# Performance work log

Measured on AMD Instinct MI355X. Metric: run time of the kernel, lower is better.

Reference implementation:

```python
import jax, jax.numpy as jnp
import numpy as np
from jax import lax

N_NODES = 10000
N_EDGES = 320000


def setup_inputs() -> dict:
    key = jax.random.key(0)
    ks = jax.random.split(key, 7)
    B, H, N, F = 4, 24, N_NODES, 32
    hid = 64
    x = jax.random.normal(ks[0], (B, H, N, F), dtype=jnp.float32)
    mask = jax.random.uniform(ks[1], (B, H), dtype=jnp.float32)
    edge_index = jax.random.randint(ks[2], (2, N_EDGES), 0, N, dtype=jnp.int32)
    W1 = jax.random.normal(ks[3], (F + 1, hid), dtype=jnp.float32) * (1.0 / np.sqrt(F + 1))
    b1 = jax.random.normal(ks[4], (hid,), dtype=jnp.float32) * 0.02
    W2 = jax.random.normal(ks[5], (hid, F), dtype=jnp.float32) * (1.0 / np.sqrt(hid))
    b2 = jax.random.normal(ks[6], (F,), dtype=jnp.float32) * 0.02
    return {"x": x, "mask": mask, "edge_index": edge_index,
            "W1": W1, "b1": b1, "W2": W2, "b2": b2}


def _gcn_norm(edge_index, num_nodes):
    # PyG GCNConv default: add self loops, symmetric normalization.
    loops = jnp.arange(num_nodes, dtype=edge_index.dtype)
    src = jnp.concatenate([edge_index[0], loops])
    dst = jnp.concatenate([edge_index[1], loops])
    deg = jax.ops.segment_sum(jnp.ones_like(dst, dtype=jnp.float32), dst,
                              num_segments=num_nodes)
    dinv = jnp.where(deg > 0, lax.rsqrt(jnp.maximum(deg, 1e-12)), 0.0)
    norm = dinv[src] * dinv[dst]  # [E']
    return src, dst, norm


def reference(x, mask, edge_index, W1, b1, W2, b2):
    B, H, N, F = x.shape
    src, dst, norm = _gcn_norm(edge_index, N)

    def gcn(h, W, b):
        # h: [B, N, Fin] -> lin, then normalized neighbor aggregation, then bias
        hw = h @ W                                   # [B, N, Fout]
        msg = hw[:, src, :].transpose(1, 0, 2)       # [E', B, Fout]
        msg = msg * norm[:, None, None]
        agg = jax.ops.segment_sum(msg, dst, num_segments=N)  # [N, B, Fout]
        return agg.transpose(1, 0, 2) + b

    def per_hour(carry, inp):
        xh, mh = inp                                 # xh: [B, N, F], mh: [B]
        mc = jnp.broadcast_to(mh[:, None, None], (B, N, 1))
        h = jnp.concatenate([xh, mc], axis=-1)       # [B, N, F+1]
        out = jnp.tanh(gcn(gcn(h, W1, b1), W2, b2))  # [B, N, F]
        return carry, out

    _, outs = lax.scan(per_hour, None,
                       (x.transpose(1, 0, 2, 3), mask.T))  # [H, B, N, F]
    return outs.transpose(1, 0, 2, 3)                     # [B, H, N, F]
```

## Files before the change

### kernel.cpp

```cpp
#include <hip/hip_runtime.h>
#include <hip/hip_fp16.h>

#define NN 10000
#define FF 32
#define PG 4
#define NGRP 24

typedef __attribute__((ext_vector_type(2))) float f32x2;

__device__ __forceinline__ unsigned short f2h(float f){
  union { unsigned short s; _Float16 h; } c; c.h = (_Float16)f; return c.s;
}

__device__ __forceinline__ void fmix2p(float& ax, float& ay, unsigned wpk, unsigned h){
  asm("v_fma_mix_f32 %0, %2, %3, %0 op_sel_hi:[1,1,0]\n\t"
      "v_fma_mix_f32 %1, %2, %3, %1 op_sel:[0,1,0] op_sel_hi:[1,1,0]"
      : "+v"(ax), "+v"(ay) : "s"(wpk), "v"(h));
}
__device__ __forceinline__ void fmix2s(float& ax, float& ay, float w, unsigned h){
  asm("v_fma_mix_f32 %0, %2, %3, %0 op_sel_hi:[0,1,0]\n\t"
      "v_fma_mix_f32 %1, %2, %3, %1 op_sel:[0,1,0] op_sel_hi:[0,1,0]"
      : "+v"(ax), "+v"(ay) : "s"(w), "v"(h));
}

__device__ __forceinline__ void pkfma(f32x2& acc, f32x2 w, f32x2 x){
  asm("v_pk_fma_f32 %0, %1, %2, %0" : "+v"(acc) : "s"(w), "v"(x));
}

__global__ void k_count(const int* __restrict__ dst, int* __restrict__ cnt,
                        unsigned* __restrict__ csr, int csrcap, int E){
  int e = blockIdx.x * 256 + threadIdx.x;
  if (e >= E) return;
  csr[e] = 0u;
  int e2 = e + E;
  if (e2 < csrcap) csr[e2] = 0u;
  atomicAdd(&cnt[dst[e]], 1);
}

__global__ __launch_bounds__(256) void k_prep(const int* __restrict__ cnt,
    int2* __restrict__ oe, float* __restrict__ dinv, int* __restrict__ gtop,
    const float* __restrict__ W1, const float* __restrict__ W2,
    const float* __restrict__ b1, float* __restrict__ W12, float* __restrict__ bb){
  int bx = blockIdx.x, tid = threadIdx.x;
  if (bx < 40){
    int i = bx * 256 + tid;
    if (i < NN){
      int c = cnt[i];
      int pad = (c + 3) & ~3;
      int start = atomicAdd(gtop, pad);
      oe[i] = make_int2(start, start + pad);
      dinv[i] = rsqrtf((float)(c + 1));
    }
  } else {
    int j = (bx - 40) * 256 + tid;
    if (j < 33 * 32){
      int k = j >> 5, c = j & 31;
      float s = 0.f;
      for (int m = 0; m < 64; ++m) s += W1[k * 64 + m] * W2[m * 32 + c];
      W12[j] = s;
    } else if (j < 33 * 32 + 32){
      int c = j - 33 * 32;
      float s = 0.f;
      for (int m = 0; m < 64; ++m) s += b1[m] * W2[m * 32 + c];
      bb[c] = s;
    }
  }
}

__global__ void k_scatter(const int* __restrict__ ei, const int2* __restrict__ oe,
                          int* __restrict__ cur, const float* __restrict__ dinv,
                          unsigned* __restrict__ csr, float* __restrict__ srow, int E){
  int e = blockIdx.x * 256 + threadIdx.x;
  if (e >= E) return;
  int s = ei[e], d = ei[E + e];
  float ds = dinv[s];
  int pos = oe[d].x + atomicAdd(&cur[d], 1);
  csr[pos] = ((unsigned)s << 16) | (unsigned)f2h(ds);
  atomicAdd(&srow[d], ds);
}

__global__ __launch_bounds__(256) void k_gemm1(const float* __restrict__ x,
    const float* __restrict__ mask, const float* __restrict__ W12,
    unsigned* __restrict__ hw){
  __shared__ float xs[256][32];
  const int pg = blockIdx.y;
  const int n0 = blockIdx.x * 256;
  const int t  = threadIdx.x;
  const int l  = t & 63;
  const int wv = __builtin_amdgcn_readfirstlane(t) >> 6;
  const int grp = pg >> 2, p = pg & 3;
  const float mv = mask[pg];
  const f32x2* Wp = (const f32x2*)W12;
  f32x2 acc[16];
  #pragma unroll
  for (int qf = 0; qf < 16; ++qf){
    f32x2 w = Wp[32 * 16 + qf];
    acc[qf].x = mv * w.x; acc[qf].y = mv * w.y;
  }
  const int rsub = l >> 3;
  const int qd   = (l & 7) ^ rsub;
  const float* xpg = x + (size_t)pg * (NN * FF);
  #pragma unroll
  for (int i = 0; i < 8; ++i){
    int chunk = wv * 8 + i;
    int grow = n0 + chunk * 8 + rsub;
    grow = grow < NN ? grow : NN - 1;
    const float* gsrc = xpg + (size_t)grow * FF + (qd << 2);
    char* ldst = (char*)&xs[0][0] + (chunk << 10);
    __builtin_amdgcn_global_load_lds(
        (const __attribute__((address_space(1))) void*)gsrc,
        (__attribute__((address_space(3))) void*)ldst, 16, 0, 0);
  }
  asm volatile("s_waitcnt vmcnt(0)" ::: "memory");
  __syncthreads();
  const int n = n0 + t;
  if (n >= NN) return;
  const int sw = (t & 7) << 2;
  #pragma unroll
  for (int Q = 0; Q < 8; ++Q){
    float4 v = *(const float4*)&xs[t][(Q << 2) ^ sw];
    const float* vf = (const float*)&v;
    #pragma unroll
    for (int j = 0; j < 4; ++j){
      int k = (Q << 2) + j;
      f32x2 xk2; xk2.x = vf[j]; xk2.y = vf[j];
      #pragma unroll
      for (int qf = 0; qf < 16; ++qf) pkfma(acc[qf], Wp[k * 16 + qf], xk2);
    }
  }
  unsigned* hwg = hw + (size_t)grp * (NN * 64) + ((size_t)n << 6) + (p << 4);
  #pragma unroll
  for (int j = 0; j < 4; ++j){
    uint4 u;
    u.x = (unsigned)f2h(acc[4*j+0].x) | ((unsigned)f2h(acc[4*j+0].y) << 16);
    u.y = (unsigned)f2h(acc[4*j+1].x) | ((unsigned)f2h(acc[4*j+1].y) << 16);
    u.z = (unsigned)f2h(acc[4*j+2].x) | ((unsigned)f2h(acc[4*j+2].y) << 16);
    u.w = (unsigned)f2h(acc[4*j+3].x) | ((unsigned)f2h(acc[4*j+3].y) << 16);
    ((uint4*)hwg)[j] = u;
  }
}

__device__ __forceinline__ void map_block(int bx, int& grp, int& chunk){
  int r  = bx / 5000;
  int w8 = bx % 5000;
  grp   = r * 8 + (w8 & 7);
  chunk = w8 >> 3;
}

#define ROWB(w) ((((unsigned)(w)) >> 8) & 0xFFFF00u)
__device__ __forceinline__ void agg_edges(int e0, int e1,
    const unsigned* __restrict__ csr, const char* __restrict__ Vb, int loff,
    float& ax, float& ay){
  int nq = (e1 - e0) >> 2;
  if (nq <= 0) return;
  const int4* c4 = (const int4*)(csr + e0);
  const int qlast = nq - 1;
  #define VLD(w) (*(const unsigned*)(Vb + (unsigned)(ROWB(w) + loff)))
  int4 cA, cB, cC, cD;
  int4 cA2, cB2, cC2, cD2;
  int4 cA3, cB3, cC3, cD3;
  unsigned rA0,rA1,rA2,rA3, rB0,rB1,rB2,rB3;
  unsigned rC0,rC1,rC2,rC3, rD0,rD1,rD2,rD3;
  {
    int i1 = 1<=qlast?1:qlast, i2 = 2<=qlast?2:qlast, i3 = 3<=qlast?3:qlast;
    cA = c4[0]; cB = c4[i1]; cC = c4[i2]; cD = c4[i3];
    int i4 = 4<=qlast?4:qlast, i5 = 5<=qlast?5:qlast;
    int i6 = 6<=qlast?6:qlast, i7 = 7<=qlast?7:qlast;
    cA2 = c4[i4]; cB2 = c4[i5]; cC2 = c4[i6]; cD2 = c4[i7];
    int i8 = 8<=qlast?8:qlast, i9 = 9<=qlast?9:qlast;
    int i10 = 10<=qlast?10:qlast, i11 = 11<=qlast?11:qlast;
    cA3 = c4[i8]; cB3 = c4[i9]; cC3 = c4[i10]; cD3 = c4[i11];
    rA0 = VLD(cA.x); rA1 = VLD(cA.y); rA2 = VLD(cA.z); rA3 = VLD(cA.w);
    rB0 = VLD(cB.x); rB1 = VLD(cB.y); rB2 = VLD(cB.z); rB3 = VLD(cB.w);
    rC0 = VLD(cC.x); rC1 = VLD(cC.y); rC2 = VLD(cC.z); rC3 = VLD(cC.w);
    rD0 = VLD(cD.x); rD1 = VLD(cD.y); rD2 = VLD(cD.z); rD3 = VLD(cD.w);
  }
  int q = 0;
  #define AGG_STEP(cX, cX2, cX3, r0, r1, r2, r3)                        \
    do {                                                                \
      fmix2p(ax, ay, (unsigned)cX.x, r0);                               \
      fmix2p(ax, ay, (unsigned)cX.y, r1);                               \
      fmix2p(ax, ay, (unsigned)cX.z, r2);                               \
      fmix2p(ax, ay, (unsigned)cX.w, r3);                               \
      r0 = VLD(cX2.x); r1 = VLD(cX2.y);                                 \
      r2 = VLD(cX2.z); r3 = VLD(cX2.w);                                 \
      cX = cX2; cX2 = cX3;                                              \
    } while (0)
  for (; q + 3 < nq; q += 4){
    AGG_STEP(cA, cA2, cA3, rA0,rA1,rA2,rA3);
    AGG_STEP(cB, cB2, cB3, rB0,rB1,rB2,rB3);
    AGG_STEP(cC, cC2, cC3, rC0,rC1,rC2,rC3);
    AGG_STEP(cD, cD2, cD3, rD0,rD1,rD2,rD3);
    int j0 = q+12 <= qlast ? q+12 : qlast;
    int j1 = q+13 <= qlast ? q+13 : qlast;
    int j2 = q+14 <= qlast ? q+14 : qlast;
    int j3 = q+15 <= qlast ? q+15 : qlast;
    cA3 = c4[j0]; cB3 = c4[j1]; cC3 = c4[j2]; cD3 = c4[j3];
  }
  #undef AGG_STEP
  #undef VLD
  int rem = nq - q;
  if (rem > 0){
    fmix2p(ax, ay, (unsigned)cA.x, rA0);
    fmix2p(ax, ay, (unsigned)cA.y, rA1);
    fmix2p(ax, ay, (unsigned)cA.z, rA2);
    fmix2p(ax, ay, (unsigned)cA.w, rA3);
  }
  if (rem > 1){
    fmix2p(ax, ay, (unsigned)cB.x, rB0);
    fmix2p(ax, ay, (unsigned)cB.y, rB1);
    fmix2p(ax, ay, (unsigned)cB.z, rB2);
    fmix2p(ax, ay, (unsigned)cB.w, rB3);
  }
  if (rem > 2){
    fmix2p(ax, ay, (unsigned)cC.x, rC0);
    fmix2p(ax, ay, (unsigned)cC.y, rC1);
    fmix2p(ax, ay, (unsigned)cC.z, rC2);
    fmix2p(ax, ay, (unsigned)cC.w, rC3);
  }
}

__global__ __launch_bounds__(256) void k_agg1(const int2* __restrict__ oe,
    const unsigned* __restrict__ csr, const float* __restrict__ dinv,
    const unsigned int* __restrict__ V, unsigned int* __restrict__ T){
  int grp, chunk; map_block(blockIdx.x, grp, chunk);
  int tid = threadIdx.x;
  int l = tid & 63;
  int wv = __builtin_amdgcn_readfirstlane(tid) >> 6;
  const char* Vb = (const char*)(V + (size_t)grp * (NN * 64));
  unsigned int* Tg = T + (size_t)grp * (NN * 64);
  int loff = l * 4;
  for (int it = 0; it < 4; ++it){
    int n = chunk * 16 + wv * 4 + it;
    float din = dinv[n];
    int2 ee = oe[n];
    unsigned sv = *(const unsigned*)(Vb + (unsigned)((n << 8) + loff));
    float ax = 0.f, ay = 0.f;
    fmix2s(ax, ay, din, sv);
    agg_edges(ee.x, ee.y, csr, Vb, loff, ax, ay);
    Tg[((size_t)n << 6) + l] =
        (unsigned)f2h(din * ax) | ((unsigned)f2h(din * ay) << 16);
  }
}

__global__ __launch_bounds__(256) void k_agg2(const int2* __restrict__ oe,
    const unsigned* __restrict__ csr, const float* __restrict__ dinv,
    const float* __restrict__ srow, const float* __restrict__ bb,
    const float* __restrict__ b2, const unsigned int* __restrict__ V,
    float* __restrict__ out){
  int grp, chunk; map_block(blockIdx.x, grp, chunk);
  int tid = threadIdx.x;
  int l = tid & 63;
  int wv = __builtin_amdgcn_readfirstlane(tid) >> 6;
  int p = l >> 4, fi = l & 15;
  const char* Vb = (const char*)(V + (size_t)grp * (NN * 64));
  int pg = grp * PG + p;
  float2 bbq = ((const float2*)bb)[fi];
  float2 b2q = ((const float2*)b2)[fi];
  float* outp = out + (size_t)pg * (NN * FF);
  int loff = l * 4;
  for (int it = 0; it < 4; ++it){
    int n = chunk * 16 + wv * 4 + it;
    float din = dinv[n];
    int2 ee = oe[n];
    unsigned sv = *(const unsigned*)(Vb + (unsigned)((n << 8) + loff));
    float ax = 0.f, ay = 0.f;
    fmix2s(ax, ay, din, sv);
    agg_edges(ee.x, ee.y, csr, Vb, loff, ax, ay);
    float sr = din * (din + srow[n]);
    float2 o;
    o.x = tanhf(din * ax + sr * bbq.x + b2q.x);
    o.y = tanhf(din * ay + sr * bbq.y + b2q.y);
    ((float2*)(outp + (size_t)n * FF))[fi] = o;
  }
}

extern "C" void kernel_launch(void* const* d_in, const int* in_sizes, int n_in,
                              void* d_out, int out_size, void* d_ws, size_t ws_size,
                              hipStream_t stream){
  const float* x    = (const float*)d_in[0];
  const float* mask = (const float*)d_in[1];
  const int*   ei   = (const int*)d_in[2];
  const float* W1   = (const float*)d_in[3];
  const float* b1   = (const float*)d_in[4];
  const float* W2   = (const float*)d_in[5];
  const float* b2   = (const float*)d_in[6];
  float* out = (float*)d_out;
  const int E = in_sizes[2] / 2;
  const int CSRCAP = E + 3 * NN + 64;

  char* wsp = (char*)d_ws;
  auto alloc = [&](size_t bytes) -> char* {
    char* p = wsp; wsp += (bytes + 255) & ~(size_t)255; return p;
  };
  int*   cnt  = (int*)  alloc((size_t)NN * 4);
  int*   cur  = (int*)  alloc((size_t)NN * 4);
  float* srow = (float*)alloc((size_t)NN * 4);
  int*   gtop = (int*)  alloc(256);
  float* dinv = (float*)alloc((size_t)NN * 4);
  int2*  oe   = (int2*) alloc((size_t)NN * 8);
  float* W12  = (float*)alloc(33 * 32 * 4);
  float* bbv  = (float*)alloc(32 * 4);
  unsigned* csr = (unsigned*)alloc((size_t)CSRCAP * 4);
  const size_t per_group = (size_t)NN * 64 * 4;
  unsigned int* hw = (unsigned int*)alloc((size_t)NGRP * per_group);
  unsigned int* t1 = (unsigned int*)alloc((size_t)NGRP * per_group);

  size_t zspan = (size_t)((char*)dinv - (char*)cnt);
  hipMemsetAsync(cnt, 0, zspan, stream);
  k_count  <<<(E + 255) / 256, 256, 0, stream>>>(ei + E, cnt, csr, CSRCAP, E);
  k_prep   <<<45, 256, 0, stream>>>(cnt, oe, dinv, gtop, W1, W2, b1, W12, bbv);
  k_scatter<<<(E + 255) / 256, 256, 0, stream>>>(ei, oe, cur, dinv, csr, srow, E);

  k_gemm1<<<dim3(40, 96), 256, 0, stream>>>(x, mask, W12, hw);
  k_agg1 <<<15000, 256, 0, stream>>>(oe, csr, dinv, hw, t1);
  k_agg2 <<<15000, 256, 0, stream>>>(oe, csr, dinv, srow, bbv, b2, t1, out);
}
```

Before: 492.1 us.

## Split edge lists across wave halves with 8-byte gathers and shuffle reduction

The aggregation kernels now split each node's edge list between the two 32-lane halves of a wave. Each half handles alternating edges and each lane gathers 8 bytes (two packed half2 values) instead of 4, and the two halves are combined with a cross-lane shuffle. This halves the number of gather instructions per edge and widens each memory access. The costs are that edge weights must sit in VGPRs instead of SGPRs, there are extra shuffles, and half the lanes sit idle during the output store.

Result: slower. 600.6 us (+22.1%).

```diff
diff --git a/kernel.cpp b/kernel.cpp
--- a/kernel.cpp
+++ b/kernel.cpp
@@ -12,15 +12,15 @@
   union { unsigned short s; _Float16 h; } c; c.h = (_Float16)f; return c.s;
 }
 
-__device__ __forceinline__ void fmix2p(float& ax, float& ay, unsigned wpk, unsigned h){
+__device__ __forceinline__ void fmix2v(float& ax, float& ay, unsigned wpk, unsigned h){
   asm("v_fma_mix_f32 %0, %2, %3, %0 op_sel_hi:[1,1,0]\n\t"
       "v_fma_mix_f32 %1, %2, %3, %1 op_sel:[0,1,0] op_sel_hi:[1,1,0]"
-      : "+v"(ax), "+v"(ay) : "s"(wpk), "v"(h));
-}
-__device__ __forceinline__ void fmix2s(float& ax, float& ay, float w, unsigned h){
+      : "+v"(ax), "+v"(ay) : "v"(wpk), "v"(h));
+}
+__device__ __forceinline__ void fmix2(float& ax, float& ay, float w, unsigned h){
   asm("v_fma_mix_f32 %0, %2, %3, %0 op_sel_hi:[0,1,0]\n\t"
       "v_fma_mix_f32 %1, %2, %3, %1 op_sel:[0,1,0] op_sel_hi:[0,1,0]"
-      : "+v"(ax), "+v"(ay) : "s"(w), "v"(h));
+      : "+v"(ax), "+v"(ay) : "v"(w), "v"(h));
 }
 
 __device__ __forceinline__ void pkfma(f32x2& acc, f32x2 w, f32x2 x){
@@ -150,47 +150,53 @@
 #define ROWB(w) ((((unsigned)(w)) >> 8) & 0xFFFF00u)
 __device__ __forceinline__ void agg_edges(int e0, int e1,
     const unsigned* __restrict__ csr, const char* __restrict__ Vb, int loff,
-    float& ax, float& ay){
+    bool hi, float& ax0, float& ay0, float& ax1, float& ay1){
   int nq = (e1 - e0) >> 2;
   if (nq <= 0) return;
   const int4* c4 = (const int4*)(csr + e0);
   const int qlast = nq - 1;
-  #define VLD(w) (*(const unsigned*)(Vb + (unsigned)(ROWB(w) + loff)))
-  int4 cA, cB, cC, cD;
+  #define V2LD(w) (*(const uint2*)(Vb + (unsigned)(ROWB(w) + loff)))
   int4 cA2, cB2, cC2, cD2;
   int4 cA3, cB3, cC3, cD3;
-  unsigned rA0,rA1,rA2,rA3, rB0,rB1,rB2,rB3;
-  unsigned rC0,rC1,rC2,rC3, rD0,rD1,rD2,rD3;
+  unsigned wA0,wA1, wB0,wB1, wC0,wC1, wD0,wD1;
+  uint2 rA0,rA1, rB0,rB1, rC0,rC1, rD0,rD1;
   {
     int i1 = 1<=qlast?1:qlast, i2 = 2<=qlast?2:qlast, i3 = 3<=qlast?3:qlast;
-    cA = c4[0]; cB = c4[i1]; cC = c4[i2]; cD = c4[i3];
+    int4 cA = c4[0], cB = c4[i1], cC = c4[i2], cD = c4[i3];
+    wA0 = hi ? (unsigned)cA.y : (unsigned)cA.x;
+    wA1 = hi ? (unsigned)cA.w : (unsigned)cA.z;
+    wB0 = hi ? (unsigned)cB.y : (unsigned)cB.x;
+    wB1 = hi ? (unsigned)cB.w : (unsigned)cB.z;
+    wC0 = hi ? (unsigned)cC.y : (unsigned)cC.x;
+    wC1 = hi ? (unsigned)cC.w : (unsigned)cC.z;
+    wD0 = hi ? (unsigned)cD.y : (unsigned)cD.x;
+    wD1 = hi ? (unsigned)cD.w : (unsigned)cD.z;
+    rA0 = V2LD(wA0); rA1 = V2LD(wA1);
+    rB0 = V2LD(wB0); rB1 = V2LD(wB1);
+    rC0 = V2LD(wC0); rC1 = V2LD(wC1);
+    rD0 = V2LD(wD0); rD1 = V2LD(wD1);
     int i4 = 4<=qlast?4:qlast, i5 = 5<=qlast?5:qlast;
     int i6 = 6<=qlast?6:qlast, i7 = 7<=qlast?7:qlast;
     cA2 = c4[i4]; cB2 = c4[i5]; cC2 = c4[i6]; cD2 = c4[i7];
     int i8 = 8<=qlast?8:qlast, i9 = 9<=qlast?9:qlast;
     int i10 = 10<=qlast?10:qlast, i11 = 11<=qlast?11:qlast;
     cA3 = c4[i8]; cB3 = c4[i9]; cC3 = c4[i10]; cD3 = c4[i11];
-    rA0 = VLD(cA.x); rA1 = VLD(cA.y); rA2 = VLD(cA.z); rA3 = VLD(cA.w);
-    rB0 = VLD(cB.x); rB1 = VLD(cB.y); rB2 = VLD(cB.z); rB3 = VLD(cB.w);
-    rC0 = VLD(cC.x); rC1 = VLD(cC.y); rC2 = VLD(cC.z); rC3 = VLD(cC.w);
-    rD0 = VLD(cD.x); rD1 = VLD(cD.y); rD2 = VLD(cD.z); rD3 = VLD(cD.w);
   }
   int q = 0;
-  #define AGG_STEP(cX, cX2, cX3, r0, r1, r2, r3)                        \
+  #define AGG_STEP(w0, w1, r0, r1, cX2, cX3)                            \
     do {                                                                \
-      fmix2p(ax, ay, (unsigned)cX.x, r0);                               \
-      fmix2p(ax, ay, (unsigned)cX.y, r1);                               \
-      fmix2p(ax, ay, (unsigned)cX.z, r2);                               \
-      fmix2p(ax, ay, (unsigned)cX.w, r3);                               \
-      r0 = VLD(cX2.x); r1 = VLD(cX2.y);                                 \
-      r2 = VLD(cX2.z); r3 = VLD(cX2.w);                                 \
-      cX = cX2; cX2 = cX3;                                              \
+      fmix2v(ax0, ay0, w0, r0.x); fmix2v(ax1, ay1, w0, r0.y);           \
+      fmix2v(ax0, ay0, w1, r1.x); fmix2v(ax1, ay1, w1, r1.y);           \
+      w0 = hi ? (unsigned)cX2.y : (unsigned)cX2.x;                      \
+      w1 = hi ? (unsigned)cX2.w : (unsigned)cX2.z;                      \
+      r0 = V2LD(w0); r1 = V2LD(w1);                                     \
+      cX2 = cX3;                                                        \
     } while (0)
   for (; q + 3 < nq; q += 4){
-    AGG_STEP(cA, cA2, cA3, rA0,rA1,rA2,rA3);
-    AGG_STEP(cB, cB2, cB3, rB0,rB1,rB2,rB3);
-    AGG_STEP(cC, cC2, cC3, rC0,rC1,rC2,rC3);
-    AGG_STEP(cD, cD2, cD3, rD0,rD1,rD2,rD3);
+    AGG_STEP(wA0, wA1, rA0, rA1, cA2, cA3);
+    AGG_STEP(wB0, wB1, rB0, rB1, cB2, cB3);
+    AGG_STEP(wC0, wC1, rC0, rC1, cC2, cC3);
+    AGG_STEP(wD0, wD1, rD0, rD1, cD2, cD3);
     int j0 = q+12 <= qlast ? q+12 : qlast;
     int j1 = q+13 <= qlast ? q+13 : qlast;
     int j2 = q+14 <= qlast ? q+14 : qlast;
@@ -198,25 +204,19 @@
     cA3 = c4[j0]; cB3 = c4[j1]; cC3 = c4[j2]; cD3 = c4[j3];
   }
   #undef AGG_STEP
-  #undef VLD
+  #undef V2LD
   int rem = nq - q;
   if (rem > 0){
-    fmix2p(ax, ay, (unsigned)cA.x, rA0);
-    fmix2p(ax, ay, (unsigned)cA.y, rA1);
-    fmix2p(ax, ay, (unsigned)cA.z, rA2);
-    fmix2p(ax, ay, (unsigned)cA.w, rA3);
+    fmix2v(ax0, ay0, wA0, rA0.x); fmix2v(ax1, ay1, wA0, rA0.y);
+    fmix2v(ax0, ay0, wA1, rA1.x); fmix2v(ax1, ay1, wA1, rA1.y);
   }
   if (rem > 1){
-    fmix2p(ax, ay, (unsigned)cB.x, rB0);
-    fmix2p(ax, ay, (unsigned)cB.y, rB1);
-    fmix2p(ax, ay, (unsigned)cB.z, rB2);
-    fmix2p(ax, ay, (unsigned)cB.w, rB3);
+    fmix2v(ax0, ay0, wB0, rB0.x); fmix2v(ax1, ay1, wB0, rB0.y);
+    fmix2v(ax0, ay0, wB1, rB1.x); fmix2v(ax1, ay1, wB1, rB1.y);
   }
   if (rem > 2){
-    fmix2p(ax, ay, (unsigned)cC.x, rC0);
-    fmix2p(ax, ay, (unsigned)cC.y, rC1);
-    fmix2p(ax, ay, (unsigned)cC.z, rC2);
-    fmix2p(ax, ay, (unsigned)cC.w, rC3);
+    fmix2v(ax0, ay0, wC0, rC0.x); fmix2v(ax1, ay1, wC0, rC0.y);
+    fmix2v(ax0, ay0, wC1, rC1.x); fmix2v(ax1, ay1, wC1, rC1.y);
   }
 }
 
@@ -225,21 +225,30 @@
     const unsigned int* __restrict__ V, unsigned int* __restrict__ T){
   int grp, chunk; map_block(blockIdx.x, grp, chunk);
   int tid = threadIdx.x;
-  int l = tid & 63;
+  int l = tid & 63, j = l & 31;
+  bool hi = l >= 32;
   int wv = __builtin_amdgcn_readfirstlane(tid) >> 6;
   const char* Vb = (const char*)(V + (size_t)grp * (NN * 64));
   unsigned int* Tg = T + (size_t)grp * (NN * 64);
-  int loff = l * 4;
+  int loff = j * 8;
   for (int it = 0; it < 4; ++it){
     int n = chunk * 16 + wv * 4 + it;
     float din = dinv[n];
     int2 ee = oe[n];
-    unsigned sv = *(const unsigned*)(Vb + (unsigned)((n << 8) + loff));
-    float ax = 0.f, ay = 0.f;
-    fmix2s(ax, ay, din, sv);
-    agg_edges(ee.x, ee.y, csr, Vb, loff, ax, ay);
-    Tg[((size_t)n << 6) + l] =
-        (unsigned)f2h(din * ax) | ((unsigned)f2h(din * ay) << 16);
+    uint2 sv = *(const uint2*)(Vb + (unsigned)((n << 8) + loff));
+    float ax0 = 0.f, ay0 = 0.f, ax1 = 0.f, ay1 = 0.f;
+    float wself = hi ? 0.f : din;
+    fmix2(ax0, ay0, wself, sv.x);
+    fmix2(ax1, ay1, wself, sv.y);
+    agg_edges(ee.x, ee.y, csr, Vb, loff, hi, ax0, ay0, ax1, ay1);
+    ax0 += __shfl_xor(ax0, 32); ay0 += __shfl_xor(ay0, 32);
+    ax1 += __shfl_xor(ax1, 32); ay1 += __shfl_xor(ay1, 32);
+    if (!hi){
+      uint2 u;
+      u.x = (unsigned)f2h(din * ax0) | ((unsigned)f2h(din * ay0) << 16);
+      u.y = (unsigned)f2h(din * ax1) | ((unsigned)f2h(din * ay1) << 16);
+      *(uint2*)(Tg + (((size_t)n) << 6) + (j << 1)) = u;
+    }
   }
 }
 
@@ -250,28 +259,36 @@
     float* __restrict__ out){
   int grp, chunk; map_block(blockIdx.x, grp, chunk);
   int tid = threadIdx.x;
-  int l = tid & 63;
+  int l = tid & 63, j = l & 31;
+  bool hi = l >= 32;
   int wv = __builtin_amdgcn_readfirstlane(tid) >> 6;
-  int p = l >> 4, fi = l & 15;
   const char* Vb = (const char*)(V + (size_t)grp * (NN * 64));
-  int pg = grp * PG + p;
-  float2 bbq = ((const float2*)bb)[fi];
-  float2 b2q = ((const float2*)b2)[fi];
+  float4 bb4 = ((const float4*)bb)[j & 7];
+  float4 b24 = ((const float4*)b2)[j & 7];
+  int pg = grp * PG + (j >> 3);
   float* outp = out + (size_t)pg * (NN * FF);
-  int loff = l * 4;
+  int loff = j * 8;
   for (int it = 0; it < 4; ++it){
     int n = chunk * 16 + wv * 4 + it;
     float din = dinv[n];
     int2 ee = oe[n];
-    unsigned sv = *(const unsigned*)(Vb + (unsigned)((n << 8) + loff));
-    float ax = 0.f, ay = 0.f;
-    fmix2s(ax, ay, din, sv);
-    agg_edges(ee.x, ee.y, csr, Vb, loff, ax, ay);
-    float sr = din * (din + srow[n]);
-    float2 o;
-    o.x = tanhf(din * ax + sr * bbq.x + b2q.x);
-    o.y = tanhf(din * ay + sr * bbq.y + b2q.y);
-    ((float2*)(outp + (size_t)n * FF))[fi] = o;
+    uint2 sv = *(const uint2*)(Vb + (unsigned)((n << 8) + loff));
+    float ax0 = 0.f, ay0 = 0.f, ax1 = 0.f, ay1 = 0.f;
+    float wself = hi ? 0.f : din;
+    fmix2(ax0, ay0, wself, sv.x);
+    fmix2(ax1, ay1, wself, sv.y);
+    agg_edges(ee.x, ee.y, csr, Vb, loff, hi, ax0, ay0, ax1, ay1);
+    ax0 += __shfl_xor(ax0, 32); ay0 += __shfl_xor(ay0, 32);
+    ax1 += __shfl_xor(ax1, 32); ay1 += __shfl_xor(ay1, 32);
+    if (!hi){
+      float sr = din * (din + srow[n]);
+      float4 o;
+      o.x = tanhf(din * ax0 + sr * bb4.x + b24.x);
+      o.y = tanhf(din * ay0 + sr * bb4.y + b24.y);
+      o.z = tanhf(din * ax1 + sr * bb4.z + b24.z);
+      o.w = tanhf(din * ay1 + sr * bb4.w + b24.w);
+      ((float4*)(outp + (size_t)n * FF))[j & 7] = o;
+    }
   }
 }
 
```
